# Kernel optimization log

Measured on AMD Instinct MI355X. Metric: run time of the kernel, lower is better.

## Reference

```python
import jax, jax.numpy as jnp
import numpy as np

NUM_CLASSES = 21
THRESH = 0.5
NEGPOS = 3
VAR0, VAR1 = 0.1, 0.2
FEAT = 19
N_ANCH = 9
B = 256
NUM_OBJS = 12
P = FEAT * FEAT * N_ANCH  # 3249


def make_priors():
    # 19x19 grid, 3 scales x 3 aspect ratios (1, 2, 1/2) -> 9 anchors/cell, center form
    cxy = (np.arange(FEAT, dtype=np.float32) + 0.5) / FEAT
    cx, cy = np.meshgrid(cxy, cxy, indexing='ij')  # [19,19]
    scales = np.array([0.1, 0.2, 0.35], dtype=np.float32)
    ratios = np.array([1.0, 2.0, 0.5], dtype=np.float32)
    w = (scales[:, None] * np.sqrt(ratios)[None, :]).reshape(-1)  # [9]
    h = (scales[:, None] / np.sqrt(ratios)[None, :]).reshape(-1)
    cx = np.broadcast_to(cx[:, :, None], (FEAT, FEAT, N_ANCH))
    cy = np.broadcast_to(cy[:, :, None], (FEAT, FEAT, N_ANCH))
    w = np.broadcast_to(w[None, None, :], (FEAT, FEAT, N_ANCH))
    h = np.broadcast_to(h[None, None, :], (FEAT, FEAT, N_ANCH))
    pri = np.stack([cx, cy, w, h], axis=-1).reshape(-1, 4)
    return jnp.asarray(np.clip(pri, 1e-3, 1.0))


def setup_inputs() -> dict:
    key = jax.random.key(0)
    k1, k2, k3, k4, k5 = jax.random.split(key, 5)
    loc_data = jax.random.normal(k1, (B, P, 4), dtype=jnp.float32)
    conf_data = jax.random.normal(k2, (B, P, NUM_CLASSES), dtype=jnp.float32)
    priors = make_priors()
    xy = jax.random.uniform(k3, (B, NUM_OBJS, 2), minval=0.05, maxval=0.65)
    wh = jax.random.uniform(k4, (B, NUM_OBJS, 2), minval=0.05, maxval=0.30)
    labels = jax.random.randint(k5, (B, NUM_OBJS), 0, NUM_CLASSES - 1).astype(jnp.float32)
    targets = jnp.concatenate([xy, xy + wh, labels[..., None]], axis=-1)  # [B,O,5]
    return {"loc_data": loc_data, "conf_data": conf_data, "priors": priors, "targets": targets}


def point_form(boxes):  # (cx,cy,w,h) -> (x1,y1,x2,y2)
    return jnp.concatenate([boxes[:, :2] - boxes[:, 2:] / 2,
                            boxes[:, :2] + boxes[:, 2:] / 2], axis=1)


def jaccard(a, b):  # a: [n,4], b: [m,4] point form -> [n,m]
    lt = jnp.maximum(a[:, None, :2], b[None, :, :2])
    rb = jnp.minimum(a[:, None, 2:], b[None, :, 2:])
    inter = jnp.prod(jnp.clip(rb - lt, 0.0, None), axis=-1)
    area_a = jnp.prod(a[:, 2:] - a[:, :2], axis=-1)
    area_b = jnp.prod(b[:, 2:] - b[:, :2], axis=-1)
    return inter / (area_a[:, None] + area_b[None, :] - inter)


def encode(matched, priors):  # matched point-form [P,4], priors center-form [P,4]
    g_cxcy = ((matched[:, :2] + matched[:, 2:]) / 2 - priors[:, :2]) / (VAR0 * priors[:, 2:])
    g_wh = jnp.log((matched[:, 2:] - matched[:, :2]) / priors[:, 2:]) / VAR1
    return jnp.concatenate([g_cxcy, g_wh], axis=1)


def match_one(truths, labels, priors, priors_pt):
    overlaps = jaccard(truths, priors_pt)          # [O,P]
    best_prior_idx = jnp.argmax(overlaps, axis=1)  # [O]
    best_truth_ov = jnp.max(overlaps, axis=0)      # [P]
    best_truth_idx = jnp.argmax(overlaps, axis=0)  # [P]
    best_truth_ov = best_truth_ov.at[best_prior_idx].set(2.0)
    best_truth_idx = best_truth_idx.at[best_prior_idx].set(jnp.arange(truths.shape[0]))
    matches = truths[best_truth_idx]               # [P,4]
    conf = labels[best_truth_idx] + 1
    conf = jnp.where(best_truth_ov < THRESH, 0, conf)
    return encode(matches, priors), conf


def reference(loc_data, conf_data, priors, targets):
    truths = targets[:, :, :4]
    labels = targets[:, :, 4].astype(jnp.int32)
    priors_pt = point_form(priors)
    loc_t, conf_t = jax.vmap(lambda t, l: match_one(t, l, priors, priors_pt))(truths, labels)
    loc_t = jax.lax.stop_gradient(loc_t)
    conf_t = jax.lax.stop_gradient(conf_t)

    pos = conf_t > 0                                               # [B,P]
    # smooth L1 (sum) over matched priors
    d = loc_data - loc_t
    ad = jnp.abs(d)
    sl1 = jnp.where(ad < 1.0, 0.5 * d * d, ad - 0.5)
    loss_l = jnp.sum(sl1 * pos[..., None].astype(sl1.dtype))

    # per-prior CE = logsumexp - logit[target]
    lse = jax.nn.logsumexp(conf_data, axis=-1)                     # [B,P]
    gathered = jnp.take_along_axis(conf_data, conf_t[..., None], axis=2)[..., 0]
    ce = lse - gathered                                            # [B,P]

    # hard negative mining: double argsort rank of neg losses
    loss_c_mine = jnp.where(pos, 0.0, ce)
    loss_idx = jnp.argsort(-loss_c_mine, axis=1)
    idx_rank = jnp.argsort(loss_idx, axis=1)
    num_pos = jnp.sum(pos, axis=1, keepdims=True)                  # [B,1]
    num_neg = jnp.minimum(NEGPOS * num_pos, P - 1)
    neg = idx_rank < num_neg

    sel = pos | neg
    loss_c = jnp.sum(jnp.where(sel, ce, 0.0))

    have_centerloss = jnp.max(sel.reshape(B, FEAT, FEAT, N_ANCH), axis=3).reshape(-1)
    conf_t_featuremap = jnp.max(conf_t.reshape(B, FEAT, FEAT, N_ANCH), axis=3).reshape(-1)

    N = jnp.sum(num_pos).astype(loc_data.dtype)
    return loss_l / N, loss_c / N, conf_t_featuremap, have_centerloss
```

## Files before the change

### kernel.cpp

```cpp
#include <hip/hip_runtime.h>
#include <math.h>

#pragma clang fp contract(off)

#define BB      256
#define PP      3249
#define NCLS    21
#define NOBJ    12
#define CELLS   361
#define THRESH_ 0.5f

typedef float vf4 __attribute__((ext_vector_type(4), aligned(4)));


__global__ __launch_bounds__(1024) void fused_kernel(
    const float* __restrict__ loc, const float* __restrict__ conf,
    const float* __restrict__ priors, const float* __restrict__ targets,
    int* __restrict__ numpos, double* __restrict__ lossl,
    double* __restrict__ lossc, float* __restrict__ out)
{
    const int b = blockIdx.x, tid = threadIdx.x;
    const int lane = tid & 63, wid = tid >> 6;

    __shared__ float s_tx1[NOBJ], s_ty1[NOBJ], s_tx2[NOBJ], s_ty2[NOBJ];
    __shared__ float s_area_t[NOBJ];
    __shared__ int   s_label[NOBJ];
    __shared__ float s_bov[PP];
    __shared__ short s_bidx[PP];
    __shared__ int   s_bpi[NOBJ];
    __shared__ float s_wov[NOBJ][16];
    __shared__ int   s_widx[NOBJ][16];
    __shared__ unsigned long long s_key[PP];
    __shared__ unsigned char s_ct[PP];
    __shared__ unsigned char s_sel[PP];
    __shared__ int s_hist[256];
    __shared__ int s_chosen, s_knext, s_nneg;
    __shared__ double s_pl[16];
    __shared__ int    s_pn[16];
    __shared__ double s_pc[16];

    if (tid < NOBJ) {
        const float* t = targets + ((size_t)b * NOBJ + tid) * 5;
        float x1 = t[0], y1 = t[1], x2 = t[2], y2 = t[3];
        s_tx1[tid] = x1; s_ty1[tid] = y1; s_tx2[tid] = x2; s_ty2[tid] = y2;
        s_label[tid] = (int)t[4];
        s_area_t[tid] = (x2 - x1) * (y2 - y1);
    }
    __syncthreads();

    float l_bov[NOBJ];
    int   l_bidx[NOBJ];
#pragma unroll
    for (int j = 0; j < NOBJ; ++j) { l_bov[j] = -1.0f; l_bidx[j] = 0x7FFFFFFF; }

    for (int p = tid; p < PP; p += 1024) {
        float cx = priors[4*p+0], cy = priors[4*p+1], w = priors[4*p+2], h = priors[4*p+3];
        float px1 = cx - w / 2.0f, py1 = cy - h / 2.0f;
        float px2 = cx + w / 2.0f, py2 = cy + h / 2.0f;
        float area_p = (px2 - px1) * (py2 - py1);
        float bov = -1.0f; int bidx = 0;
#pragma unroll
        for (int j = 0; j < NOBJ; ++j) {
            float ltx = fmaxf(s_tx1[j], px1);
            float lty = fmaxf(s_ty1[j], py1);
            float rbx = fminf(s_tx2[j], px2);
            float rby = fminf(s_ty2[j], py2);
            float iw = fmaxf(rbx - ltx, 0.0f);
            float ih = fmaxf(rby - lty, 0.0f);
            float inter = iw * ih;
            float iou = inter / ((s_area_t[j] + area_p) - inter);
            if (iou > bov) { bov = iou; bidx = j; }
            if (iou > l_bov[j]) { l_bov[j] = iou; l_bidx[j] = p; }
        }
        s_bov[p] = bov;
        s_bidx[p] = (short)bidx;
    }

#pragma unroll
    for (int j = 0; j < NOBJ; ++j) {
        float ov = l_bov[j]; int ix = l_bidx[j];
#pragma unroll
        for (int off = 32; off > 0; off >>= 1) {
            float ov2 = __shfl_xor(ov, off);
            int   ix2 = __shfl_xor(ix, off);
            if (ov2 > ov || (ov2 == ov && ix2 < ix)) { ov = ov2; ix = ix2; }
        }
        if (lane == 0) { s_wov[j][wid] = ov; s_widx[j][wid] = ix; }
    }
    __syncthreads();
    if (tid < NOBJ) {
        float ov = s_wov[tid][0]; int ix = s_widx[tid][0];
#pragma unroll
        for (int w2 = 1; w2 < 16; ++w2) {
            float ov2 = s_wov[tid][w2]; int ix2 = s_widx[tid][w2];
            if (ov2 > ov || (ov2 == ov && ix2 < ix)) { ov = ov2; ix = ix2; }
        }
        s_bpi[tid] = ix;
    }
    __syncthreads();

    int my_pos = 0;
    double my_lossl = 0.0;
    const float* confb = conf + (size_t)b * PP * NCLS;
    for (int p = tid; p < PP; p += 1024) {
        int jov = -1;
#pragma unroll
        for (int j = 0; j < NOBJ; ++j) if (s_bpi[j] == p) jov = j;
        int idx; float ov;
        if (jov >= 0) { idx = jov; ov = 2.0f; }
        else          { idx = (int)s_bidx[p]; ov = s_bov[p]; }
        int c = (ov < THRESH_) ? 0 : (s_label[idx] + 1);
        s_ct[p] = (unsigned char)c;

        const float* cd = confb + (size_t)p * NCLS;
        const vf4* cd4 = (const vf4*)cd;
        float rw[NCLS];
#pragma unroll
        for (int v = 0; v < 5; ++v) {
            vf4 q = cd4[v];
            rw[4*v+0] = q[0]; rw[4*v+1] = q[1]; rw[4*v+2] = q[2]; rw[4*v+3] = q[3];
        }
        rw[20] = cd[20];

        float m = rw[0];
#pragma unroll
        for (int k = 1; k < NCLS; ++k) m = fmaxf(m, rw[k]);
        float s = 0.0f;
#pragma unroll
        for (int k = 0; k < NCLS; ++k) s += expf(rw[k] - m);
        float cdc = rw[0];
#pragma unroll
        for (int k = 1; k < NCLS; ++k) if (c == k) cdc = rw[k];
        float ce = (logf(s) + m) - cdc;

        float v = (c > 0) ? 0.0f : ce;
        s_key[p] = ((unsigned long long)__float_as_uint(v) << 32)
                 | (unsigned int)(0xFFFFFFFFu - (unsigned int)p);
        s_bov[p] = ce;

        if (c > 0) {
            ++my_pos;
            float cx = priors[4*p+0], cy = priors[4*p+1], w = priors[4*p+2], h = priors[4*p+3];
            float m0 = s_tx1[idx], m1 = s_ty1[idx], m2 = s_tx2[idx], m3 = s_ty2[idx];
            float g0 = ((m0 + m2) / 2.0f - cx) / (0.1f * w);
            float g1 = ((m1 + m3) / 2.0f - cy) / (0.1f * h);
            float g2 = logf((m2 - m0) / w) / 0.2f;
            float g3 = logf((m3 - m1) / h) / 0.2f;
            const float* ld = loc + ((size_t)b * PP + p) * 4;
            float d0 = ld[0] - g0, d1 = ld[1] - g1, d2 = ld[2] - g2, d3 = ld[3] - g3;
            float a0 = fabsf(d0), a1 = fabsf(d1), a2 = fabsf(d2), a3 = fabsf(d3);
            my_lossl += (double)((a0 < 1.0f) ? 0.5f * d0 * d0 : a0 - 0.5f);
            my_lossl += (double)((a1 < 1.0f) ? 0.5f * d1 * d1 : a1 - 0.5f);
            my_lossl += (double)((a2 < 1.0f) ? 0.5f * d2 * d2 : a2 - 0.5f);
            my_lossl += (double)((a3 < 1.0f) ? 0.5f * d3 * d3 : a3 - 0.5f);
        }
    }
#pragma unroll
    for (int off = 32; off > 0; off >>= 1) {
        my_lossl += __shfl_down(my_lossl, off);
        my_pos   += __shfl_down(my_pos, off);
    }
    if (lane == 0) { s_pl[wid] = my_lossl; s_pn[wid] = my_pos; }
    __syncthreads();
    if (tid == 0) {
        double L = 0.0; int n = 0;
#pragma unroll
        for (int w2 = 0; w2 < 16; ++w2) { L += s_pl[w2]; n += s_pn[w2]; }
        lossl[b] = L; numpos[b] = n;
        s_nneg = min(3 * n, PP - 1);
    }
    __syncthreads();

    const int ds[6] = {56, 48, 40, 32, 8, 0};
    unsigned long long prefix = 0ull, pmask = 0ull;
    int kk = s_nneg;
#pragma unroll
    for (int ri = 0; ri < 6; ++ri) {
        const int d = ds[ri];
        if (tid < 256) s_hist[tid] = 0;
        __syncthreads();
        for (int i = tid; i < PP; i += 1024) {
            unsigned long long key = s_key[i];
            if ((key & pmask) == prefix)
                atomicAdd(&s_hist[(int)((key >> d) & 0xFF)], 1);
        }
        __syncthreads();
        if (tid < 64) {
            int h0 = s_hist[4*lane+0], h1 = s_hist[4*lane+1];
            int h2 = s_hist[4*lane+2], h3 = s_hist[4*lane+3];
            int ls = h0 + h1 + h2 + h3;
            int x = ls;
#pragma unroll
            for (int off = 1; off < 64; off <<= 1) {
                int y = __shfl_down(x, off);
                if (lane + off < 64) x += y;
            }
            int excl = x - ls;
            int cb3 = excl;
            int cb2 = cb3 + h3;
            int cb1 = cb2 + h2;
            int cb0 = cb1 + h1;
            if (cb3 < kk && kk <= cb3 + h3) { s_chosen = 4*lane+3; s_knext = kk - cb3; }
            if (cb2 < kk && kk <= cb2 + h2) { s_chosen = 4*lane+2; s_knext = kk - cb2; }
            if (cb1 < kk && kk <= cb1 + h1) { s_chosen = 4*lane+1; s_knext = kk - cb1; }
            if (cb0 < kk && kk <= cb0 + h0) { s_chosen = 4*lane+0; s_knext = kk - cb0; }
        }
        __syncthreads();
        prefix |= ((unsigned long long)(unsigned int)s_chosen) << d;
        pmask  |= 0xFFull << d;
        kk = s_knext;
        if (d == 32) { prefix |= 0xFFFF0000ull; pmask |= 0xFFFF0000ull; }
        __syncthreads();
    }
    const unsigned long long kth = prefix;

    double my_c = 0.0;
    for (int p = tid; p < PP; p += 1024) {
        int c = s_ct[p];
        bool sel = (c > 0) || (s_key[p] >= kth);
        s_sel[p] = sel ? 1 : 0;
        if (sel) my_c += (double)s_bov[p];
    }
    __syncthreads();

    for (int cI = tid; cI < CELLS; cI += 1024) {
        int mc = 0, hv = 0;
#pragma unroll
        for (int a = 0; a < 9; ++a) {
            int p = cI * 9 + a;
            int cv = s_ct[p];
            mc = (cv > mc) ? cv : mc;
            hv |= s_sel[p];
        }
        out[2 + (size_t)b * CELLS + cI] = (float)mc;
        out[2 + (size_t)BB * CELLS + (size_t)b * CELLS + cI] = (float)hv;
    }

#pragma unroll
    for (int off = 32; off > 0; off >>= 1) my_c += __shfl_down(my_c, off);
    if (lane == 0) s_pc[wid] = my_c;
    __syncthreads();
    if (tid == 0) {
        double L = 0.0;
#pragma unroll
        for (int w2 = 0; w2 < 16; ++w2) L += s_pc[w2];
        lossc[b] = L;
    }
}

__global__ __launch_bounds__(256) void finalize_kernel(
    const int* __restrict__ numpos, const double* __restrict__ lossl,
    const double* __restrict__ lossc, float* __restrict__ out)
{
    __shared__ double s_l[256], s_c[256];
    __shared__ int s_n[256];
    int tid = threadIdx.x;
    s_n[tid] = numpos[tid];
    s_l[tid] = lossl[tid];
    s_c[tid] = lossc[tid];
    __syncthreads();
    for (int s = 128; s > 0; s >>= 1) {
        if (tid < s) { s_n[tid] += s_n[tid + s]; s_l[tid] += s_l[tid + s]; s_c[tid] += s_c[tid + s]; }
        __syncthreads();
    }
    if (tid == 0) {
        double N = (double)s_n[0];
        out[0] = (float)(s_l[0] / N);
        out[1] = (float)(s_c[0] / N);
    }
}

extern "C" void kernel_launch(void* const* d_in, const int* in_sizes, int n_in,
                              void* d_out, int out_size, void* d_ws, size_t ws_size,
                              hipStream_t stream) {
    const float* loc     = (const float*)d_in[0];
    const float* conf    = (const float*)d_in[1];
    const float* priors  = (const float*)d_in[2];
    const float* targets = (const float*)d_in[3];
    float* out = (float*)d_out;

    double* ws_lossl  = (double*)d_ws;
    double* ws_lossc  = ws_lossl + BB;
    int*    ws_numpos = (int*)(ws_lossc + BB);

    hipLaunchKernelGGL(fused_kernel, dim3(BB), dim3(1024), 0, stream,
                       loc, conf, priors, targets, ws_numpos, ws_lossl, ws_lossc, out);
    hipLaunchKernelGGL(finalize_kernel, dim3(1), dim3(256), 0, stream,
                       ws_numpos, ws_lossl, ws_lossc, out);
}
```

Before: 139.4 us.

## Prefetch conf logits early and software-pipeline conf loads across prior loop

Each thread's first row of conf logits is now loaded before the IoU matching phase, so that global-memory latency overlaps with the matching compute. The conf loop is software-pipelined to load the next prior's row while the current one is processed. The best-prior indices are cached in registers, and launch bounds now request 4 blocks per CU. This raises register pressure, and the occupancy hint may force spills.

Measured after the change: 143.2 us. 1.03x slower.

```diff
diff --git a/kernel.cpp b/kernel.cpp
--- a/kernel.cpp
+++ b/kernel.cpp
@@ -13,7 +13,7 @@
 typedef float vf4 __attribute__((ext_vector_type(4), aligned(4)));
 
 
-__global__ __launch_bounds__(1024) void fused_kernel(
+__global__ __launch_bounds__(1024, 4) void fused_kernel(
     const float* __restrict__ loc, const float* __restrict__ conf,
     const float* __restrict__ priors, const float* __restrict__ targets,
     int* __restrict__ numpos, double* __restrict__ lossl,
@@ -48,6 +48,15 @@
     }
     __syncthreads();
 
+    const float* confb = conf + (size_t)b * PP * NCLS;
+    vf4 q[5]; float q20 = 0.0f;
+    {
+        const vf4* cd4 = (const vf4*)(confb + (size_t)tid * NCLS);
+#pragma unroll
+        for (int v = 0; v < 5; ++v) q[v] = cd4[v];
+        q20 = confb[(size_t)tid * NCLS + 20];
+    }
+
     float l_bov[NOBJ];
     int   l_bidx[NOBJ];
 #pragma unroll
@@ -99,28 +108,37 @@
     }
     __syncthreads();
 
+    int bpi[NOBJ];
+#pragma unroll
+    for (int j = 0; j < NOBJ; ++j) bpi[j] = s_bpi[j];
+
     int my_pos = 0;
     double my_lossl = 0.0;
-    const float* confb = conf + (size_t)b * PP * NCLS;
     for (int p = tid; p < PP; p += 1024) {
+        const int pn = p + 1024;
+        vf4 qn[5]; float qn20 = 0.0f;
+        if (pn < PP) {
+            const vf4* cd4n = (const vf4*)(confb + (size_t)pn * NCLS);
+#pragma unroll
+            for (int v = 0; v < 5; ++v) qn[v] = cd4n[v];
+            qn20 = confb[(size_t)pn * NCLS + 20];
+        }
+
         int jov = -1;
 #pragma unroll
-        for (int j = 0; j < NOBJ; ++j) if (s_bpi[j] == p) jov = j;
+        for (int j = 0; j < NOBJ; ++j) if (bpi[j] == p) jov = j;
         int idx; float ov;
         if (jov >= 0) { idx = jov; ov = 2.0f; }
         else          { idx = (int)s_bidx[p]; ov = s_bov[p]; }
         int c = (ov < THRESH_) ? 0 : (s_label[idx] + 1);
         s_ct[p] = (unsigned char)c;
 
-        const float* cd = confb + (size_t)p * NCLS;
-        const vf4* cd4 = (const vf4*)cd;
         float rw[NCLS];
 #pragma unroll
         for (int v = 0; v < 5; ++v) {
-            vf4 q = cd4[v];
-            rw[4*v+0] = q[0]; rw[4*v+1] = q[1]; rw[4*v+2] = q[2]; rw[4*v+3] = q[3];
-        }
-        rw[20] = cd[20];
+            rw[4*v+0] = q[v][0]; rw[4*v+1] = q[v][1]; rw[4*v+2] = q[v][2]; rw[4*v+3] = q[v][3];
+        }
+        rw[20] = q20;
 
         float m = rw[0];
 #pragma unroll
@@ -154,6 +172,10 @@
             my_lossl += (double)((a2 < 1.0f) ? 0.5f * d2 * d2 : a2 - 0.5f);
             my_lossl += (double)((a3 < 1.0f) ? 0.5f * d3 * d3 : a3 - 0.5f);
         }
+
+#pragma unroll
+        for (int v2 = 0; v2 < 5; ++v2) q[v2] = qn[v2];
+        q20 = qn20;
     }
 #pragma unroll
     for (int off = 32; off > 0; off >>= 1) {
```
